# Optimization experiments

Measured on AMD Instinct MI355X. Metric: run time of the kernel, lower is better.

The kernel has to match this reference:

```python
import jax, jax.numpy as jnp
import numpy as np

B, T, EMB = 2, 2048, 1024
H, D = 16, 64          # num_heads, head_dim; hidden = H*D = 1024
SCALE = D ** (-0.5)


def setup_inputs() -> dict:
    key = jax.random.key(0)
    k1, k2, k3, k4, k5 = jax.random.split(key, 5)
    return {
        "x":    jax.random.normal(k1, (B, T, EMB), dtype=jnp.float32),
        "Wqkv": jax.random.normal(k2, (EMB, 3 * H * D), dtype=jnp.float32) * (EMB ** -0.5),
        "bqkv": jax.random.normal(k3, (3 * H * D,), dtype=jnp.float32) * 0.02,
        "Wout": jax.random.normal(k4, (H * D, EMB), dtype=jnp.float32) * ((H * D) ** -0.5),
        "bout": jax.random.normal(k5, (EMB,), dtype=jnp.float32) * 0.02,
    }


def reference(x, Wqkv, bqkv, Wout, bout):
    b, t, _ = x.shape
    qkv = x @ Wqkv + bqkv                                   # [b, t, 3*H*D]
    q, k, v = jnp.split(qkv, 3, axis=-1)
    split_heads = lambda a: a.reshape(b, t, H, D).transpose(0, 2, 1, 3)  # [b,h,t,d]
    q, k, v = split_heads(q), split_heads(k), split_heads(v)

    scores = jnp.einsum('bhid,bhjd->bhij', q, k) * SCALE    # [b,h,t,t]
    causal = jnp.tril(jnp.ones((t, t), dtype=bool))         # lower-triangular mask
    scores = jnp.where(causal, scores, -jnp.inf)
    attn = jax.nn.softmax(scores, axis=-1)                  # dropout: eval mode (identity)

    out = jnp.einsum('bhij,bhjd->bhid', attn, v)            # [b,h,t,d]
    out = out.transpose(0, 2, 1, 3).reshape(b, t, H * D)    # [b,t,H*D]
    return out @ Wout + bout                                # [b,t,EMB]
```

## Files before the change

kernel.cpp:

```cpp
#include <hip/hip_runtime.h>
#include <hip/hip_bf16.h>

typedef __bf16 bf16x8 __attribute__((ext_vector_type(8)));
typedef float f32x4 __attribute__((ext_vector_type(4)));
typedef float f32x16 __attribute__((ext_vector_type(16)));
typedef unsigned int uint32x4v __attribute__((ext_vector_type(4)));

#define B_ 2
#define T_ 2048
#define EMB_ 1024
#define H_ 16
#define D_ 64
#define M_ (B_ * T_)
#define NQKV_ (3 * H_ * D_)

#define GPTR(p) ((const __attribute__((address_space(1))) unsigned int*)(p))
#define LPTR(p) ((__attribute__((address_space(3))) unsigned int*)(p))

__device__ __forceinline__ unsigned pk2(float a, float b) {
    unsigned short ua = __builtin_bit_cast(unsigned short, (__bf16)a);
    unsigned short ub = __builtin_bit_cast(unsigned short, (__bf16)b);
    return (unsigned)ua | ((unsigned)ub << 16);
}

__global__ void cast_bf16_k(const float* __restrict__ in, __bf16* __restrict__ out) {
    int i = (blockIdx.x * blockDim.x + threadIdx.x) * 8;
    float4 a = *reinterpret_cast<const float4*>(in + i);
    float4 b = *reinterpret_cast<const float4*>(in + i + 4);
    bf16x8 o;
    o[0] = (__bf16)a.x; o[1] = (__bf16)a.y; o[2] = (__bf16)a.z; o[3] = (__bf16)a.w;
    o[4] = (__bf16)b.x; o[5] = (__bf16)b.y; o[6] = (__bf16)b.z; o[7] = (__bf16)b.w;
    *reinterpret_cast<bf16x8*>(out + i) = o;
}

__global__ void transpose_cast_k(const float* __restrict__ in, __bf16* __restrict__ out,
                                 int K, int N) {
    __shared__ float tile[32][33];
    int bx = blockIdx.x;
    int by = blockIdx.y;
    int tx = threadIdx.x, ty = threadIdx.y;
    for (int j = 0; j < 32; j += 8)
        tile[ty + j][tx] = in[(size_t)(by * 32 + ty + j) * N + bx * 32 + tx];
    __syncthreads();
    for (int j = 0; j < 32; j += 8)
        out[(size_t)(bx * 32 + ty + j) * K + by * 32 + tx] = (__bf16)tile[tx][ty + j];
}

#define BM 128
#define BN 128
#define BK 64

template <int EPI>
__global__ __launch_bounds__(256, 2) void gemm_bf16_k(
    const __bf16* __restrict__ A, const __bf16* __restrict__ Bt,
    const float* __restrict__ bias, float* __restrict__ outF,
    __bf16* __restrict__ Qg, __bf16* __restrict__ Kg, __bf16* __restrict__ Vtg,
    int Mdim, int Ndim, int Kdim) {
    __shared__ __bf16 As[BM * BK];
    __shared__ __bf16 Bs[BN * BK];
    const int tid = threadIdx.x;
    const int lane = tid & 63;
    const int w = tid >> 6;
    const int wr = w >> 1, wc = w & 1;
    const int row0 = blockIdx.y * BM;
    const int col0 = blockIdx.x * BN;
    const int lr = lane & 15;
    const int lg = lane >> 4;

    f32x4 acc[4][4] = {};

    for (int k0 = 0; k0 < Kdim; k0 += BK) {
        #pragma unroll
        for (int i = 0; i < 4; ++i) {
            int r0 = 32 * w + 8 * i;
            int row = r0 + (lane >> 3);
            int c8 = (lane & 7) * 8;
            __builtin_amdgcn_global_load_lds(
                GPTR(A + (size_t)(row0 + row) * Kdim + k0 + c8), LPTR(&As[r0 * BK]), 16, 0, 0);
            __builtin_amdgcn_global_load_lds(
                GPTR(Bt + (size_t)(col0 + row) * Kdim + k0 + c8), LPTR(&Bs[r0 * BK]), 16, 0, 0);
        }
        __syncthreads();
        #pragma unroll
        for (int kk = 0; kk < BK; kk += 32) {
            bf16x8 af[4], bfr[4];
            #pragma unroll
            for (int mt = 0; mt < 4; ++mt)
                af[mt] = *reinterpret_cast<const bf16x8*>(&As[(wr * 64 + mt * 16 + lr) * BK + kk + lg * 8]);
            #pragma unroll
            for (int nt = 0; nt < 4; ++nt)
                bfr[nt] = *reinterpret_cast<const bf16x8*>(&Bs[(wc * 64 + nt * 16 + lr) * BK + kk + lg * 8]);
            #pragma unroll
            for (int mt = 0; mt < 4; ++mt)
                #pragma unroll
                for (int nt = 0; nt < 4; ++nt)
                    acc[mt][nt] = __builtin_amdgcn_mfma_f32_16x16x32_bf16(
                        af[mt], bfr[nt], acc[mt][nt], 0, 0, 0);
        }
        __syncthreads();
    }

    #pragma unroll
    for (int mt = 0; mt < 4; ++mt)
        #pragma unroll
        for (int nt = 0; nt < 4; ++nt)
            #pragma unroll
            for (int r = 0; r < 4; ++r) {
                int row = row0 + wr * 64 + mt * 16 + lg * 4 + r;
                int col = col0 + wc * 64 + nt * 16 + lr;
                float v = acc[mt][nt][r] + bias[col];
                if (EPI == 0) {
                    outF[(size_t)row * Ndim + col] = v;
                } else {
                    int part = col >> 10;
                    int hh = (col >> 6) & 15;
                    int dd = col & 63;
                    int bb = row >> 11;
                    int tt = row & 2047;
                    __bf16 bv = (__bf16)v;
                    size_t bh = (size_t)(bb * H_ + hh);
                    if (part == 0)
                        Qg[(bh * T_ + tt) * D_ + dd] = bv;
                    else if (part == 1)
                        Kg[(bh * T_ + tt) * D_ + dd] = bv;
                    else
                        Vtg[(bh * D_ + dd) * T_ + tt] = bv;
                }
            }
}

#define KVB 64

__global__ __launch_bounds__(256, 2) void attn_k(
    const __bf16* __restrict__ Qg, const __bf16* __restrict__ Kg,
    const __bf16* __restrict__ Vtg, __bf16* __restrict__ Og) {
    __shared__ __bf16 Ks[KVB * 64];
    __shared__ __bf16 Vs[64 * 64];

    const int tid = threadIdx.x;
    const int lane = tid & 63;
    const int w = tid >> 6;
    const int l31 = lane & 31;
    const int hi = lane >> 5;

    const int id = blockIdx.x;
    const int bh = id & 31;
    const int qb = (id < 256) ? (15 - (id >> 5)) : ((id - 256) >> 5);
    const size_t baseQK = (size_t)bh * T_ * D_;
    const size_t baseVt = (size_t)bh * D_ * T_;
    const int qw = qb * 128 + w * 32;
    const int q_lane = qw + l31;

    bf16x8 qf[4];
    #pragma unroll
    for (int ks = 0; ks < 4; ++ks)
        qf[ks] = *reinterpret_cast<const bf16x8*>(
            &Qg[baseQK + (size_t)q_lane * D_ + ks * 16 + hi * 8]);

    f32x16 o0 = {}, o1 = {};
    float m = -1e30f, lsum = 0.f;

    const int ntile = 2 * qb + 2;
    for (int t = 0; t < ntile; ++t) {
        const int kv0 = t * KVB;
        #pragma unroll
        for (int i = 0; i < 2; ++i) {
            int r0 = 16 * w + 8 * i;
            int row = r0 + (lane >> 3);
            int c = (lane & 7) ^ (row & 7);
            __builtin_amdgcn_global_load_lds(
                GPTR(Kg + baseQK + (size_t)(kv0 + row) * D_ + 8 * c),
                LPTR(&Ks[r0 * 64]), 16, 0, 0);
            __builtin_amdgcn_global_load_lds(
                GPTR(Vtg + baseVt + (size_t)row * T_ + kv0 + 8 * c),
                LPTR(&Vs[r0 * 64]), 16, 0, 0);
        }
        __syncthreads();

        if (kv0 < qw + 32) {
            f32x16 s0 = {}, s1 = {};
            #pragma unroll
            for (int ks = 0; ks < 4; ++ks) {
                int c = (((2 * ks + hi) ^ (l31 & 7)) * 8);
                bf16x8 kf0 = *reinterpret_cast<const bf16x8*>(&Ks[l31 * 64 + c]);
                bf16x8 kf1 = *reinterpret_cast<const bf16x8*>(&Ks[(32 + l31) * 64 + c]);
                s0 = __builtin_amdgcn_mfma_f32_32x32x16_bf16(kf0, qf[ks], s0, 0, 0, 0);
                s1 = __builtin_amdgcn_mfma_f32_32x32x16_bf16(kf1, qf[ks], s1, 0, 0, 0);
            }
            const bool diag = (kv0 + KVB > qw);
            if (diag) {
                #pragma unroll
                for (int r = 0; r < 16; ++r) {
                    int kvr = kv0 + (r & 3) + 8 * (r >> 2) + 4 * hi;
                    s0[r] = (kvr <= q_lane) ? s0[r] * 0.125f : -1e30f;
                    s1[r] = (kvr + 32 <= q_lane) ? s1[r] * 0.125f : -1e30f;
                }
            } else {
                #pragma unroll
                for (int r = 0; r < 16; ++r) { s0[r] *= 0.125f; s1[r] *= 0.125f; }
            }
            float pmax = -1e30f;
            #pragma unroll
            for (int r = 0; r < 16; ++r)
                pmax = fmaxf(pmax, fmaxf(s0[r], s1[r]));
            pmax = fmaxf(pmax, __shfl_xor(pmax, 32, 64));
            if (__any(pmax > m + 8.f)) {
                float mnew = fmaxf(m, pmax);
                float corr = __expf(m - mnew);
                m = mnew;
                lsum *= corr;
                #pragma unroll
                for (int r = 0; r < 16; ++r) {
                    int qsrc = (r & 3) + 8 * (r >> 2) + 4 * hi;
                    float cb = __shfl(corr, qsrc, 64);
                    o0[r] *= cb; o1[r] *= cb;
                }
            }
            float ps = 0.f;
            #pragma unroll
            for (int r = 0; r < 16; ++r) {
                s0[r] = __expf(s0[r] - m);
                s1[r] = __expf(s1[r] - m);
                ps += s0[r] + s1[r];
            }
            ps += __shfl_xor(ps, 32, 64);
            lsum += ps;
            #pragma unroll
            for (int ks = 0; ks < 4; ++ks) {
                const int e = (ks & 1) * 8;
                unsigned w0, w1, w2, w3;
                if (ks < 2) {
                    w0 = pk2(s0[e + 0], s0[e + 1]); w1 = pk2(s0[e + 2], s0[e + 3]);
                    w2 = pk2(s0[e + 4], s0[e + 5]); w3 = pk2(s0[e + 6], s0[e + 7]);
                } else {
                    w0 = pk2(s1[e + 0], s1[e + 1]); w1 = pk2(s1[e + 2], s1[e + 3]);
                    w2 = pk2(s1[e + 4], s1[e + 5]); w3 = pk2(s1[e + 6], s1[e + 7]);
                }
                unsigned pw0 = __shfl_xor(w0, 32, 64);
                unsigned pw1 = __shfl_xor(w1, 32, 64);
                unsigned pw2 = __shfl_xor(w2, 32, 64);
                unsigned pw3 = __shfl_xor(w3, 32, 64);
                uint32x4v uf;
                uf.x = hi ? pw2 : w0;
                uf.y = hi ? pw3 : w1;
                uf.z = hi ? w2 : pw0;
                uf.w = hi ? w3 : pw1;
                bf16x8 pa = __builtin_bit_cast(bf16x8, uf);
                int c = (((2 * ks + hi) ^ (l31 & 7)) * 8);
                bf16x8 vf0 = *reinterpret_cast<const bf16x8*>(&Vs[l31 * 64 + c]);
                bf16x8 vf1 = *reinterpret_cast<const bf16x8*>(&Vs[(32 + l31) * 64 + c]);
                o0 = __builtin_amdgcn_mfma_f32_32x32x16_bf16(pa, vf0, o0, 0, 0, 0);
                o1 = __builtin_amdgcn_mfma_f32_32x32x16_bf16(pa, vf1, o1, 0, 0, 0);
            }
        }
        __syncthreads();
    }

    const int b = bh >> 4, h = bh & 15;
    float li = 1.0f / lsum;
    #pragma unroll
    for (int r = 0; r < 16; ++r) {
        int qsrc = (r & 3) + 8 * (r >> 2) + 4 * hi;
        float cb = __shfl(li, qsrc, 64);
        int tt = qw + qsrc;
        size_t base = (size_t)(b * T_ + tt) * (H_ * D_) + h * D_;
        Og[base + l31]      = (__bf16)(o0[r] * cb);
        Og[base + 32 + l31] = (__bf16)(o1[r] * cb);
    }
}

extern "C" void kernel_launch(void* const* d_in, const int* in_sizes, int n_in,
                              void* d_out, int out_size, void* d_ws, size_t ws_size,
                              hipStream_t stream) {
    const float* x    = (const float*)d_in[0];
    const float* Wqkv = (const float*)d_in[1];
    const float* bqkv = (const float*)d_in[2];
    const float* Wout = (const float*)d_in[3];
    const float* bout = (const float*)d_in[4];
    float* outF = (float*)d_out;

    char* ws = (char*)d_ws;
    __bf16* xb     = (__bf16*)(ws);
    __bf16* WqkvT  = (__bf16*)(ws + 8388608);
    __bf16* WoutT  = (__bf16*)(ws + 14680064);
    __bf16* Qg     = (__bf16*)(ws + 16777216);
    __bf16* Kg     = (__bf16*)(ws + 25165824);
    __bf16* Vtg    = (__bf16*)(ws + 33554432);
    __bf16* Og     = (__bf16*)(ws + 41943040);

    cast_bf16_k<<<(M_ * EMB_) / (256 * 8), 256, 0, stream>>>(x, xb);
    transpose_cast_k<<<dim3(NQKV_ / 32, EMB_ / 32), dim3(32, 8), 0, stream>>>(Wqkv, WqkvT, EMB_, NQKV_);
    transpose_cast_k<<<dim3(EMB_ / 32, EMB_ / 32), dim3(32, 8), 0, stream>>>(Wout, WoutT, EMB_, EMB_);

    gemm_bf16_k<1><<<dim3(NQKV_ / BN, M_ / BM), 256, 0, stream>>>(
        xb, WqkvT, bqkv, nullptr, Qg, Kg, Vtg, M_, NQKV_, EMB_);

    attn_k<<<512, 256, 0, stream>>>(Qg, Kg, Vtg, Og);

    gemm_bf16_k<0><<<dim3(EMB_ / BN, M_ / BM), 256, 0, stream>>>(
        Og, WoutT, bout, outF, nullptr, nullptr, nullptr, M_, EMB_, EMB_);
}
```

Before: 208.5 us.

## Double-buffer GEMM LDS, fold softmax scale into Q, register-only single-wave attention

The GEMM now double-buffers its LDS tiles with an XOR swizzle, so the next K tile loads while the current one is computed and bank conflicts are reduced. The QKV epilogue pre-multiplies Q by scale*log2(e), which lets attention use exp2 with no per-score scaling. Attention is restructured into 2048 single-wave blocks that read K and V straight from global memory into registers with one-tile prefetch. This removes the LDS staging and block barriers, adds s_setprio hints around the MFMAs, and masks only the final diagonal tile. In exchange, each wave re-reads K/V from global/L2 with no sharing across waves, and register pressure rises.

```diff
diff --git a/kernel.cpp b/kernel.cpp
--- a/kernel.cpp
+++ b/kernel.cpp
@@ -13,6 +13,8 @@
 #define D_ 64
 #define M_ (B_ * T_)
 #define NQKV_ (3 * H_ * D_)
+
+#define QSCALE 0.18033688011112042f
 
 #define GPTR(p) ((const __attribute__((address_space(1))) unsigned int*)(p))
 #define LPTR(p) ((__attribute__((address_space(3))) unsigned int*)(p))
@@ -56,8 +58,8 @@
     const float* __restrict__ bias, float* __restrict__ outF,
     __bf16* __restrict__ Qg, __bf16* __restrict__ Kg, __bf16* __restrict__ Vtg,
     int Mdim, int Ndim, int Kdim) {
-    __shared__ __bf16 As[BM * BK];
-    __shared__ __bf16 Bs[BN * BK];
+    __shared__ __bf16 As[2][BM * BK];
+    __shared__ __bf16 Bs[2][BN * BK];
     const int tid = threadIdx.x;
     const int lane = tid & 63;
     const int w = tid >> 6;
@@ -69,27 +71,45 @@
 
     f32x4 acc[4][4] = {};
 
-    for (int k0 = 0; k0 < Kdim; k0 += BK) {
+    const int srow = 32 * w;
+    const int lrow = lane >> 3;
+    const int scc = ((lane & 7) ^ (lrow & 7)) * 8;
+
+    auto STAGE = [&](int t, int bufi) {
+        const int k0 = t * BK;
         #pragma unroll
         for (int i = 0; i < 4; ++i) {
-            int r0 = 32 * w + 8 * i;
-            int row = r0 + (lane >> 3);
-            int c8 = (lane & 7) * 8;
+            int r0 = srow + 8 * i;
+            int row = r0 + lrow;
             __builtin_amdgcn_global_load_lds(
-                GPTR(A + (size_t)(row0 + row) * Kdim + k0 + c8), LPTR(&As[r0 * BK]), 16, 0, 0);
+                GPTR(A + (size_t)(row0 + row) * Kdim + k0 + scc), LPTR(&As[bufi][r0 * BK]), 16, 0, 0);
             __builtin_amdgcn_global_load_lds(
-                GPTR(Bt + (size_t)(col0 + row) * Kdim + k0 + c8), LPTR(&Bs[r0 * BK]), 16, 0, 0);
-        }
-        __syncthreads();
+                GPTR(Bt + (size_t)(col0 + row) * Kdim + k0 + scc), LPTR(&Bs[bufi][r0 * BK]), 16, 0, 0);
+        }
+    };
+
+    const int nk = Kdim / BK;
+    STAGE(0, 0);
+    __syncthreads();
+    for (int t = 0; t < nk; ++t) {
+        if (t + 1 < nk) STAGE(t + 1, (t + 1) & 1);
+        const __bf16* __restrict__ Ab = As[t & 1];
+        const __bf16* __restrict__ Bb = Bs[t & 1];
         #pragma unroll
         for (int kk = 0; kk < BK; kk += 32) {
             bf16x8 af[4], bfr[4];
             #pragma unroll
-            for (int mt = 0; mt < 4; ++mt)
-                af[mt] = *reinterpret_cast<const bf16x8*>(&As[(wr * 64 + mt * 16 + lr) * BK + kk + lg * 8]);
+            for (int mt = 0; mt < 4; ++mt) {
+                int row = wr * 64 + mt * 16 + lr;
+                int cc = ((kk / 8 + lg) ^ (row & 7)) * 8;
+                af[mt] = *reinterpret_cast<const bf16x8*>(&Ab[row * BK + cc]);
+            }
             #pragma unroll
-            for (int nt = 0; nt < 4; ++nt)
-                bfr[nt] = *reinterpret_cast<const bf16x8*>(&Bs[(wc * 64 + nt * 16 + lr) * BK + kk + lg * 8]);
+            for (int nt = 0; nt < 4; ++nt) {
+                int row = wc * 64 + nt * 16 + lr;
+                int cc = ((kk / 8 + lg) ^ (row & 7)) * 8;
+                bfr[nt] = *reinterpret_cast<const bf16x8*>(&Bb[row * BK + cc]);
+            }
             #pragma unroll
             for (int mt = 0; mt < 4; ++mt)
                 #pragma unroll
@@ -117,39 +137,107 @@
                     int dd = col & 63;
                     int bb = row >> 11;
                     int tt = row & 2047;
-                    __bf16 bv = (__bf16)v;
                     size_t bh = (size_t)(bb * H_ + hh);
                     if (part == 0)
-                        Qg[(bh * T_ + tt) * D_ + dd] = bv;
+                        Qg[(bh * T_ + tt) * D_ + dd] = (__bf16)(v * QSCALE);
                     else if (part == 1)
-                        Kg[(bh * T_ + tt) * D_ + dd] = bv;
+                        Kg[(bh * T_ + tt) * D_ + dd] = (__bf16)v;
                     else
-                        Vtg[(bh * D_ + dd) * T_ + tt] = bv;
+                        Vtg[(bh * D_ + dd) * T_ + tt] = (__bf16)v;
                 }
             }
 }
 
 #define KVB 64
 
-__global__ __launch_bounds__(256, 2) void attn_k(
+template <bool MASK>
+__device__ __forceinline__ void attn_tile(
+    const bf16x8 (&qf)[4], const bf16x8 (&k0)[4], const bf16x8 (&k1)[4],
+    const bf16x8 (&v0)[4], const bf16x8 (&v1)[4],
+    f32x16& o0, f32x16& o1, float& m, float& lsum, int thr, int hi) {
+    f32x16 s0 = {}, s1 = {};
+    __builtin_amdgcn_s_setprio(1);
+    #pragma unroll
+    for (int ks = 0; ks < 4; ++ks) {
+        s0 = __builtin_amdgcn_mfma_f32_32x32x16_bf16(k0[ks], qf[ks], s0, 0, 0, 0);
+        s1 = __builtin_amdgcn_mfma_f32_32x32x16_bf16(k1[ks], qf[ks], s1, 0, 0, 0);
+    }
+    __builtin_amdgcn_s_setprio(0);
+    if (MASK) {
+        #pragma unroll
+        for (int r = 0; r < 16; ++r) {
+            int c = (r & 3) + 8 * (r >> 2);
+            if (c > thr) s0[r] = -1e30f;
+            if (c + 32 > thr) s1[r] = -1e30f;
+        }
+    }
+    float pmax = -1e30f;
+    #pragma unroll
+    for (int r = 0; r < 16; ++r) pmax = fmaxf(pmax, fmaxf(s0[r], s1[r]));
+    pmax = fmaxf(pmax, __shfl_xor(pmax, 32, 64));
+    if (__any(pmax > m + 8.f)) {
+        float mnew = fmaxf(m, pmax);
+        float corr = __builtin_exp2f(m - mnew);
+        m = mnew;
+        lsum *= corr;
+        #pragma unroll
+        for (int r = 0; r < 16; ++r) {
+            int qsrc = (r & 3) + 8 * (r >> 2) + 4 * hi;
+            float cb = __shfl(corr, qsrc, 64);
+            o0[r] *= cb; o1[r] *= cb;
+        }
+    }
+    float ps = 0.f;
+    #pragma unroll
+    for (int r = 0; r < 16; ++r) {
+        s0[r] = __builtin_exp2f(s0[r] - m);
+        s1[r] = __builtin_exp2f(s1[r] - m);
+        ps += s0[r] + s1[r];
+    }
+    ps += __shfl_xor(ps, 32, 64);
+    lsum += ps;
+    #pragma unroll
+    for (int ks = 0; ks < 4; ++ks) {
+        const int e = (ks & 1) * 8;
+        unsigned w0, w1, w2, w3;
+        if (ks < 2) {
+            w0 = pk2(s0[e + 0], s0[e + 1]); w1 = pk2(s0[e + 2], s0[e + 3]);
+            w2 = pk2(s0[e + 4], s0[e + 5]); w3 = pk2(s0[e + 6], s0[e + 7]);
+        } else {
+            w0 = pk2(s1[e + 0], s1[e + 1]); w1 = pk2(s1[e + 2], s1[e + 3]);
+            w2 = pk2(s1[e + 4], s1[e + 5]); w3 = pk2(s1[e + 6], s1[e + 7]);
+        }
+        unsigned pw0 = __shfl_xor(w0, 32, 64);
+        unsigned pw1 = __shfl_xor(w1, 32, 64);
+        unsigned pw2 = __shfl_xor(w2, 32, 64);
+        unsigned pw3 = __shfl_xor(w3, 32, 64);
+        uint32x4v uf;
+        uf.x = hi ? pw2 : w0;
+        uf.y = hi ? pw3 : w1;
+        uf.z = hi ? w2 : pw0;
+        uf.w = hi ? w3 : pw1;
+        bf16x8 pa = __builtin_bit_cast(bf16x8, uf);
+        __builtin_amdgcn_s_setprio(1);
+        o0 = __builtin_amdgcn_mfma_f32_32x32x16_bf16(pa, v0[ks], o0, 0, 0, 0);
+        o1 = __builtin_amdgcn_mfma_f32_32x32x16_bf16(pa, v1[ks], o1, 0, 0, 0);
+        __builtin_amdgcn_s_setprio(0);
+    }
+}
+
+__global__ __launch_bounds__(64, 2) void attn_k(
     const __bf16* __restrict__ Qg, const __bf16* __restrict__ Kg,
     const __bf16* __restrict__ Vtg, __bf16* __restrict__ Og) {
-    __shared__ __bf16 Ks[KVB * 64];
-    __shared__ __bf16 Vs[64 * 64];
-
-    const int tid = threadIdx.x;
-    const int lane = tid & 63;
-    const int w = tid >> 6;
+    const int lane = threadIdx.x;
     const int l31 = lane & 31;
     const int hi = lane >> 5;
-
-    const int id = blockIdx.x;
-    const int bh = id & 31;
-    const int qb = (id < 256) ? (15 - (id >> 5)) : ((id - 256) >> 5);
+    const int bid = blockIdx.x;
+    const int bh = bid & 31;
+    const int qt = 63 - (bid >> 5);
+    const int q0 = qt * 32;
+    const int q_lane = q0 + l31;
+    const int nt = (qt >> 1) + 1;
     const size_t baseQK = (size_t)bh * T_ * D_;
     const size_t baseVt = (size_t)bh * D_ * T_;
-    const int qw = qb * 128 + w * 32;
-    const int q_lane = qw + l31;
 
     bf16x8 qf[4];
     #pragma unroll
@@ -157,103 +245,46 @@
         qf[ks] = *reinterpret_cast<const bf16x8*>(
             &Qg[baseQK + (size_t)q_lane * D_ + ks * 16 + hi * 8]);
 
+    const __bf16* kp0 = Kg + baseQK + (size_t)l31 * D_ + hi * 8;
+    const __bf16* kp1 = kp0 + 32 * D_;
+    const __bf16* vp0 = Vtg + baseVt + (size_t)l31 * T_ + hi * 8;
+
     f32x16 o0 = {}, o1 = {};
     float m = -1e30f, lsum = 0.f;
 
-    const int ntile = 2 * qb + 2;
-    for (int t = 0; t < ntile; ++t) {
-        const int kv0 = t * KVB;
-        #pragma unroll
-        for (int i = 0; i < 2; ++i) {
-            int r0 = 16 * w + 8 * i;
-            int row = r0 + (lane >> 3);
-            int c = (lane & 7) ^ (row & 7);
-            __builtin_amdgcn_global_load_lds(
-                GPTR(Kg + baseQK + (size_t)(kv0 + row) * D_ + 8 * c),
-                LPTR(&Ks[r0 * 64]), 16, 0, 0);
-            __builtin_amdgcn_global_load_lds(
-                GPTR(Vtg + baseVt + (size_t)row * T_ + kv0 + 8 * c),
-                LPTR(&Vs[r0 * 64]), 16, 0, 0);
-        }
-        __syncthreads();
-
-        if (kv0 < qw + 32) {
-            f32x16 s0 = {}, s1 = {};
-            #pragma unroll
-            for (int ks = 0; ks < 4; ++ks) {
-                int c = (((2 * ks + hi) ^ (l31 & 7)) * 8);
-                bf16x8 kf0 = *reinterpret_cast<const bf16x8*>(&Ks[l31 * 64 + c]);
-                bf16x8 kf1 = *reinterpret_cast<const bf16x8*>(&Ks[(32 + l31) * 64 + c]);
-                s0 = __builtin_amdgcn_mfma_f32_32x32x16_bf16(kf0, qf[ks], s0, 0, 0, 0);
-                s1 = __builtin_amdgcn_mfma_f32_32x32x16_bf16(kf1, qf[ks], s1, 0, 0, 0);
-            }
-            const bool diag = (kv0 + KVB > qw);
-            if (diag) {
-                #pragma unroll
-                for (int r = 0; r < 16; ++r) {
-                    int kvr = kv0 + (r & 3) + 8 * (r >> 2) + 4 * hi;
-                    s0[r] = (kvr <= q_lane) ? s0[r] * 0.125f : -1e30f;
-                    s1[r] = (kvr + 32 <= q_lane) ? s1[r] * 0.125f : -1e30f;
-                }
-            } else {
-                #pragma unroll
-                for (int r = 0; r < 16; ++r) { s0[r] *= 0.125f; s1[r] *= 0.125f; }
-            }
-            float pmax = -1e30f;
-            #pragma unroll
-            for (int r = 0; r < 16; ++r)
-                pmax = fmaxf(pmax, fmaxf(s0[r], s1[r]));
-            pmax = fmaxf(pmax, __shfl_xor(pmax, 32, 64));
-            if (__any(pmax > m + 8.f)) {
-                float mnew = fmaxf(m, pmax);
-                float corr = __expf(m - mnew);
-                m = mnew;
-                lsum *= corr;
-                #pragma unroll
-                for (int r = 0; r < 16; ++r) {
-                    int qsrc = (r & 3) + 8 * (r >> 2) + 4 * hi;
-                    float cb = __shfl(corr, qsrc, 64);
-                    o0[r] *= cb; o1[r] *= cb;
-                }
-            }
-            float ps = 0.f;
-            #pragma unroll
-            for (int r = 0; r < 16; ++r) {
-                s0[r] = __expf(s0[r] - m);
-                s1[r] = __expf(s1[r] - m);
-                ps += s0[r] + s1[r];
-            }
-            ps += __shfl_xor(ps, 32, 64);
-            lsum += ps;
-            #pragma unroll
-            for (int ks = 0; ks < 4; ++ks) {
-                const int e = (ks & 1) * 8;
-                unsigned w0, w1, w2, w3;
-                if (ks < 2) {
-                    w0 = pk2(s0[e + 0], s0[e + 1]); w1 = pk2(s0[e + 2], s0[e + 3]);
-                    w2 = pk2(s0[e + 4], s0[e + 5]); w3 = pk2(s0[e + 6], s0[e + 7]);
-                } else {
-                    w0 = pk2(s1[e + 0], s1[e + 1]); w1 = pk2(s1[e + 2], s1[e + 3]);
-                    w2 = pk2(s1[e + 4], s1[e + 5]); w3 = pk2(s1[e + 6], s1[e + 7]);
-                }
-                unsigned pw0 = __shfl_xor(w0, 32, 64);
-                unsigned pw1 = __shfl_xor(w1, 32, 64);
-                unsigned pw2 = __shfl_xor(w2, 32, 64);
-                unsigned pw3 = __shfl_xor(w3, 32, 64);
-                uint32x4v uf;
-                uf.x = hi ? pw2 : w0;
-                uf.y = hi ? pw3 : w1;
-                uf.z = hi ? w2 : pw0;
-                uf.w = hi ? w3 : pw1;
-                bf16x8 pa = __builtin_bit_cast(bf16x8, uf);
-                int c = (((2 * ks + hi) ^ (l31 & 7)) * 8);
-                bf16x8 vf0 = *reinterpret_cast<const bf16x8*>(&Vs[l31 * 64 + c]);
-                bf16x8 vf1 = *reinterpret_cast<const bf16x8*>(&Vs[(32 + l31) * 64 + c]);
-                o0 = __builtin_amdgcn_mfma_f32_32x32x16_bf16(pa, vf0, o0, 0, 0, 0);
-                o1 = __builtin_amdgcn_mfma_f32_32x32x16_bf16(pa, vf1, o1, 0, 0, 0);
-            }
-        }
-        __syncthreads();
+    bf16x8 ka0[4], ka1[4];
+    #pragma unroll
+    for (int ks = 0; ks < 4; ++ks) {
+        ka0[ks] = *reinterpret_cast<const bf16x8*>(kp0 + ks * 16);
+        ka1[ks] = *reinterpret_cast<const bf16x8*>(kp1 + ks * 16);
+    }
+
+    for (int t = 0; t < nt - 1; ++t) {
+        bf16x8 v0[4], v1[4], kn0[4], kn1[4];
+        const __bf16* vt = vp0 + t * KVB;
+        const __bf16* kt = kp0 + (size_t)(t + 1) * KVB * D_;
+        #pragma unroll
+        for (int ks = 0; ks < 4; ++ks) {
+            v0[ks] = *reinterpret_cast<const bf16x8*>(vt + ks * 16);
+            v1[ks] = *reinterpret_cast<const bf16x8*>(vt + (size_t)32 * T_ + ks * 16);
+            kn0[ks] = *reinterpret_cast<const bf16x8*>(kt + ks * 16);
+            kn1[ks] = *reinterpret_cast<const bf16x8*>(kt + 32 * D_ + ks * 16);
+        }
+        attn_tile<false>(qf, ka0, ka1, v0, v1, o0, o1, m, lsum, 0, hi);
+        #pragma unroll
+        for (int ks = 0; ks < 4; ++ks) { ka0[ks] = kn0[ks]; ka1[ks] = kn1[ks]; }
+    }
+    {
+        const int t = nt - 1;
+        bf16x8 v0[4], v1[4];
+        const __bf16* vt = vp0 + t * KVB;
+        #pragma unroll
+        for (int ks = 0; ks < 4; ++ks) {
+            v0[ks] = *reinterpret_cast<const bf16x8*>(vt + ks * 16);
+            v1[ks] = *reinterpret_cast<const bf16x8*>(vt + (size_t)32 * T_ + ks * 16);
+        }
+        attn_tile<true>(qf, ka0, ka1, v0, v1, o0, o1, m, lsum,
+                        q_lane - t * KVB - 4 * hi, hi);
     }
 
     const int b = bh >> 4, h = bh & 15;
@@ -262,7 +293,7 @@
     for (int r = 0; r < 16; ++r) {
         int qsrc = (r & 3) + 8 * (r >> 2) + 4 * hi;
         float cb = __shfl(li, qsrc, 64);
-        int tt = qw + qsrc;
+        int tt = q0 + qsrc;
         size_t base = (size_t)(b * T_ + tt) * (H_ * D_) + h * D_;
         Og[base + l31]      = (__bf16)(o0[r] * cb);
         Og[base + 32 + l31] = (__bf16)(o1[r] * cb);
@@ -295,7 +326,7 @@
     gemm_bf16_k<1><<<dim3(NQKV_ / BN, M_ / BM), 256, 0, stream>>>(
         xb, WqkvT, bqkv, nullptr, Qg, Kg, Vtg, M_, NQKV_, EMB_);
 
-    attn_k<<<512, 256, 0, stream>>>(Qg, Kg, Vtg, Og);
+    attn_k<<<2048, 64, 0, stream>>>(Qg, Kg, Vtg, Og);
 
     gemm_bf16_k<0><<<dim3(EMB_ / BN, M_ / BM), 256, 0, stream>>>(
         Og, WoutT, bout, outF, nullptr, nullptr, nullptr, M_, EMB_, EMB_);
```

After: 239.0 us. +14.6%, slower.
